# Kernel tuning notes

Measured on AMD Instinct MI355X. Metric: run time of the kernel, lower is better.

Reference implementation:

```python
import jax, jax.numpy as jnp
import numpy as np

N_ATOMS = 10000
N_PAIRS = 500000
N_DESC = 64


def setup_inputs() -> dict:
    key = jax.random.key(0)
    k = jax.random.split(key, 6)
    stdv = float(np.sqrt(6.0 / 3.0))  # matches reset_parameters uniform bound
    return {
        "coeffs": jax.random.normal(k[0], (1, N_ATOMS, N_DESC), dtype=jnp.float32),
        "coeffs_derivs": jax.random.normal(k[1], (1, 3, N_PAIRS, N_DESC), dtype=jnp.float32),
        "w1": jax.random.uniform(k[2], (N_DESC,), jnp.float32, -stdv, stdv),
        "b1": jnp.zeros((N_DESC,), jnp.float32),
        "w_last": jax.random.uniform(k[3], (N_DESC,), jnp.float32, -stdv, stdv),
        "b_last": jnp.zeros((1,), jnp.float32),
        "central_atom_index": jax.random.randint(k[4], (N_PAIRS,), 0, N_ATOMS, dtype=jnp.int32),
        "neigh_atom_index": jax.random.randint(k[5], (N_PAIRS,), 0, N_ATOMS, dtype=jnp.int32),
    }


def reference(coeffs, coeffs_derivs, w1, b1, w_last, b_last,
              central_atom_index, neigh_atom_index):
    # coeffs: [1, N, D]; coeffs_derivs: [1, 3, P, D]
    num_atoms = coeffs.shape[1]
    e_pa = jnp.tanh(coeffs * w1 + b1)            # [1, N, D]
    dfdw = 1.0 - e_pa * e_pa                     # tanh' chain, [1, N, D]
    # gather per-pair central-atom derivative, broadcast over 3 force dims
    f = dfdw[:, central_atom_index, :][:, None, :, :] * (coeffs_derivs * w1)  # [1,3,P,D]
    energy = jnp.sum(e_pa * w_last) / num_atoms + b_last   # [1]
    f = -jnp.sum(f * w_last, axis=3)             # [1, 3, P]
    # scatter-sum pair forces onto neighbor atoms (replaces O(n^2) python loop)
    out_f = jnp.zeros((1, 3, num_atoms), dtype=f.dtype).at[:, :, neigh_atom_index].add(f)
    return energy, out_f
```

## Files before the change

### kernel.cpp

```cpp
#include <hip/hip_runtime.h>

#define N_ATOMS 10000
#define N_PAIRS 500000
#define N_DESC  64

__global__ void init_out_kernel(float* __restrict__ out,
                                const float* __restrict__ b_last,
                                int out_size) {
    int i = blockIdx.x * blockDim.x + threadIdx.x;
    if (i < out_size) out[i] = (i == 0) ? b_last[0] : 0.0f;
}

__global__ void atom_kernel(const float* __restrict__ coeffs,
                            const float* __restrict__ w1,
                            const float* __restrict__ b1,
                            const float* __restrict__ w_last,
                            float* __restrict__ g,
                            float* __restrict__ out) {
    const int i = blockIdx.x * blockDim.x + threadIdx.x;
    const int d = i & (N_DESC - 1);

    const float wd = w1[d];
    const float wl = w_last[d];
    const float e  = tanhf(coeffs[i] * wd + b1[d]);

    g[i] = (1.0f - e * e) * wd * wl;

    float epart = e * wl * (1.0f / (float)N_ATOMS);

    #pragma unroll
    for (int off = 32; off > 0; off >>= 1)
        epart += __shfl_down(epart, off, 64);

    __shared__ float smem[4];
    const int lane = threadIdx.x & 63;
    const int wv   = threadIdx.x >> 6;
    if (lane == 0) smem[wv] = epart;
    __syncthreads();
    if (threadIdx.x == 0) {
        atomicAdd(out, smem[0] + smem[1] + smem[2] + smem[3]);
    }
}

__global__ void __launch_bounds__(256)
pair_kernel(const float4* __restrict__ cd4,
            const float4* __restrict__ g4,
            const int*   __restrict__ central,
            const int*   __restrict__ neigh,
            float* __restrict__ out_f) {
    const int tid = blockIdx.x * blockDim.x + threadIdx.x;
    const int p   = tid >> 4;
    const int l   = tid & 15;
    if (p >= N_PAIRS) return;

    const int c = central[p];
    const float4 gv = g4[c * 16 + l];

    const size_t plane4 = (size_t)N_PAIRS * 16;
    const float4* base = cd4 + (size_t)p * 16 + l;
    const float4 b0 = base[0];
    const float4 b1v = base[plane4];
    const float4 b2 = base[2 * plane4];

    float s0 = gv.x * b0.x  + gv.y * b0.y  + gv.z * b0.z  + gv.w * b0.w;
    float s1 = gv.x * b1v.x + gv.y * b1v.y + gv.z * b1v.z + gv.w * b1v.w;
    float s2 = gv.x * b2.x  + gv.y * b2.y  + gv.z * b2.z  + gv.w * b2.w;

    #pragma unroll
    for (int m = 8; m > 0; m >>= 1) {
        s0 += __shfl_xor(s0, m, 64);
        s1 += __shfl_xor(s1, m, 64);
        s2 += __shfl_xor(s2, m, 64);
    }

    if (l == 0) {
        const int nb = neigh[p];
        atomicAdd(&out_f[nb],               -s0);
        atomicAdd(&out_f[N_ATOMS + nb],     -s1);
        atomicAdd(&out_f[2 * N_ATOMS + nb], -s2);
    }
}

extern "C" void kernel_launch(void* const* d_in, const int* in_sizes, int n_in,
                              void* d_out, int out_size, void* d_ws, size_t ws_size,
                              hipStream_t stream) {
    const float* coeffs  = (const float*)d_in[0];
    const float* cd      = (const float*)d_in[1];
    const float* w1      = (const float*)d_in[2];
    const float* b1      = (const float*)d_in[3];
    const float* w_last  = (const float*)d_in[4];
    const float* b_last  = (const float*)d_in[5];
    const int*   central = (const int*)d_in[6];
    const int*   neigh   = (const int*)d_in[7];

    float* out = (float*)d_out;
    float* g   = (float*)d_ws;

    {
        int blocks = (out_size + 255) / 256;
        init_out_kernel<<<blocks, 256, 0, stream>>>(out, b_last, out_size);
    }

    {
        int total  = N_ATOMS * N_DESC;
        int blocks = total / 256;
        atom_kernel<<<blocks, 256, 0, stream>>>(coeffs, w1, b1, w_last, g, out);
    }

    {
        long long total_threads = (long long)N_PAIRS * 16;
        int blocks = (int)((total_threads + 255) / 256);
        pair_kernel<<<blocks, 256, 0, stream>>>(
            (const float4*)cd, (const float4*)g, central, neigh, out + 1);
    }
}
```

Measured before the change: 546.7 us.

## Fuse output init into atom kernel, process two pairs per thread, spread atomics

Drops the separate init kernel: the atom kernel zeroes the force buffer and writes per-block energy partials to workspace, and the pair kernel's block 0 reduces those partials deterministically. Each 16-lane group now handles two pairs (p and p+P/2) with nontemporal streaming loads, giving more memory-level parallelism per thread. The three atomic adds per pair are spread across different lanes. The aim is less launch overhead, less cache pollution from the large derivative stream, and more loads in flight, at the cost of fewer threads and more registers.

New measurement: 510.5 us. 1.07x faster.

```diff
diff --git a/kernel.cpp b/kernel.cpp
--- a/kernel.cpp
+++ b/kernel.cpp
@@ -3,20 +3,26 @@
 #define N_ATOMS 10000
 #define N_PAIRS 500000
 #define N_DESC  64
+#define HALF_PAIRS (N_PAIRS / 2)
+#define ATOM_BLOCKS (N_ATOMS * N_DESC / 256)
+#define FORCE_ELEMS (3 * N_ATOMS)
 
-__global__ void init_out_kernel(float* __restrict__ out,
-                                const float* __restrict__ b_last,
-                                int out_size) {
-    int i = blockIdx.x * blockDim.x + threadIdx.x;
-    if (i < out_size) out[i] = (i == 0) ? b_last[0] : 0.0f;
-}
+#define WS_EPART_OFF (N_ATOMS * N_DESC)
 
-__global__ void atom_kernel(const float* __restrict__ coeffs,
-                            const float* __restrict__ w1,
-                            const float* __restrict__ b1,
-                            const float* __restrict__ w_last,
-                            float* __restrict__ g,
-                            float* __restrict__ out) {
+typedef float f4 __attribute__((ext_vector_type(4)));
+
+__global__ void __launch_bounds__(256)
+atom_kernel(const float* __restrict__ coeffs,
+            const float* __restrict__ w1,
+            const float* __restrict__ b1,
+            const float* __restrict__ w_last,
+            float* __restrict__ ws,
+            float* __restrict__ out) {
+    if (blockIdx.x < 118) {
+        int j = blockIdx.x * 256 + threadIdx.x;
+        if (j < FORCE_ELEMS) out[1 + j] = 0.0f;
+    }
+
     const int i = blockIdx.x * blockDim.x + threadIdx.x;
     const int d = i & (N_DESC - 1);
 
@@ -24,10 +30,9 @@
     const float wl = w_last[d];
     const float e  = tanhf(coeffs[i] * wd + b1[d]);
 
-    g[i] = (1.0f - e * e) * wd * wl;
+    ws[i] = (1.0f - e * e) * wd * wl;
 
     float epart = e * wl * (1.0f / (float)N_ATOMS);
-
     #pragma unroll
     for (int off = 32; off > 0; off >>= 1)
         epart += __shfl_down(epart, off, 64);
@@ -37,47 +42,82 @@
     const int wv   = threadIdx.x >> 6;
     if (lane == 0) smem[wv] = epart;
     __syncthreads();
-    if (threadIdx.x == 0) {
-        atomicAdd(out, smem[0] + smem[1] + smem[2] + smem[3]);
-    }
+    if (threadIdx.x == 0)
+        ws[WS_EPART_OFF + blockIdx.x] = smem[0] + smem[1] + smem[2] + smem[3];
 }
 
 __global__ void __launch_bounds__(256)
-pair_kernel(const float4* __restrict__ cd4,
-            const float4* __restrict__ g4,
-            const int*   __restrict__ central,
-            const int*   __restrict__ neigh,
-            float* __restrict__ out_f) {
+pair_kernel(const f4* __restrict__ cd4,
+            const f4* __restrict__ g4,
+            const float*  __restrict__ ws,
+            const float*  __restrict__ b_last,
+            const int*    __restrict__ central,
+            const int*    __restrict__ neigh,
+            float* __restrict__ out) {
+    if (blockIdx.x == 0 && threadIdx.x < 64) {
+        float s = 0.0f;
+        for (int idx = threadIdx.x; idx < ATOM_BLOCKS; idx += 64)
+            s += ws[WS_EPART_OFF + idx];
+        #pragma unroll
+        for (int off = 32; off > 0; off >>= 1)
+            s += __shfl_down(s, off, 64);
+        if (threadIdx.x == 0) out[0] = s + b_last[0];
+    }
+
+    float* __restrict__ out_f = out + 1;
+
     const int tid = blockIdx.x * blockDim.x + threadIdx.x;
-    const int p   = tid >> 4;
+    const int grp = tid >> 4;
     const int l   = tid & 15;
-    if (p >= N_PAIRS) return;
+    if (grp >= HALF_PAIRS) return;
 
-    const int c = central[p];
-    const float4 gv = g4[c * 16 + l];
+    const int pA = grp;
+    const int pB = grp + HALF_PAIRS;
+
+    const int cA = central[pA];
+    const int cB = central[pB];
+    const int nA = neigh[pA];
+    const int nB = neigh[pB];
 
     const size_t plane4 = (size_t)N_PAIRS * 16;
-    const float4* base = cd4 + (size_t)p * 16 + l;
-    const float4 b0 = base[0];
-    const float4 b1v = base[plane4];
-    const float4 b2 = base[2 * plane4];
+    const f4* baseA = cd4 + (size_t)pA * 16 + l;
+    const f4* baseB = cd4 + (size_t)pB * 16 + l;
 
-    float s0 = gv.x * b0.x  + gv.y * b0.y  + gv.z * b0.z  + gv.w * b0.w;
-    float s1 = gv.x * b1v.x + gv.y * b1v.y + gv.z * b1v.z + gv.w * b1v.w;
-    float s2 = gv.x * b2.x  + gv.y * b2.y  + gv.z * b2.z  + gv.w * b2.w;
+    const f4 a0 = __builtin_nontemporal_load(baseA);
+    const f4 a1 = __builtin_nontemporal_load(baseA + plane4);
+    const f4 a2 = __builtin_nontemporal_load(baseA + 2 * plane4);
+    const f4 c0 = __builtin_nontemporal_load(baseB);
+    const f4 c1 = __builtin_nontemporal_load(baseB + plane4);
+    const f4 c2 = __builtin_nontemporal_load(baseB + 2 * plane4);
+    const f4 gA = g4[cA * 16 + l];
+    const f4 gB = g4[cB * 16 + l];
+
+    float sA0 = gA.x * a0.x + gA.y * a0.y + gA.z * a0.z + gA.w * a0.w;
+    float sA1 = gA.x * a1.x + gA.y * a1.y + gA.z * a1.z + gA.w * a1.w;
+    float sA2 = gA.x * a2.x + gA.y * a2.y + gA.z * a2.z + gA.w * a2.w;
+    float sB0 = gB.x * c0.x + gB.y * c0.y + gB.z * c0.z + gB.w * c0.w;
+    float sB1 = gB.x * c1.x + gB.y * c1.y + gB.z * c1.z + gB.w * c1.w;
+    float sB2 = gB.x * c2.x + gB.y * c2.y + gB.z * c2.z + gB.w * c2.w;
 
     #pragma unroll
     for (int m = 8; m > 0; m >>= 1) {
-        s0 += __shfl_xor(s0, m, 64);
-        s1 += __shfl_xor(s1, m, 64);
-        s2 += __shfl_xor(s2, m, 64);
+        sA0 += __shfl_xor(sA0, m, 64);
+        sA1 += __shfl_xor(sA1, m, 64);
+        sA2 += __shfl_xor(sA2, m, 64);
+        sB0 += __shfl_xor(sB0, m, 64);
+        sB1 += __shfl_xor(sB1, m, 64);
+        sB2 += __shfl_xor(sB2, m, 64);
     }
 
     if (l == 0) {
-        const int nb = neigh[p];
-        atomicAdd(&out_f[nb],               -s0);
-        atomicAdd(&out_f[N_ATOMS + nb],     -s1);
-        atomicAdd(&out_f[2 * N_ATOMS + nb], -s2);
+        atomicAdd(&out_f[nA], -sA0);
+        atomicAdd(&out_f[nB], -sB0);
+    } else if (l == 4) {
+        atomicAdd(&out_f[N_ATOMS + nA], -sA1);
+        atomicAdd(&out_f[N_ATOMS + nB], -sB1);
+    } else if (l == 8) {
+        atomicAdd(&out_f[2 * N_ATOMS + nA], -sA2);
+        atomicAdd(&out_f[2 * N_ATOMS + nB], -sB2);
     }
 }
 
@@ -94,23 +134,14 @@
     const int*   neigh   = (const int*)d_in[7];
 
     float* out = (float*)d_out;
-    float* g   = (float*)d_ws;
+    float* ws  = (float*)d_ws;
+
+    atom_kernel<<<ATOM_BLOCKS, 256, 0, stream>>>(coeffs, w1, b1, w_last, ws, out);
 
     {
-        int blocks = (out_size + 255) / 256;
-        init_out_kernel<<<blocks, 256, 0, stream>>>(out, b_last, out_size);
-    }
-
-    {
-        int total  = N_ATOMS * N_DESC;
-        int blocks = total / 256;
-        atom_kernel<<<blocks, 256, 0, stream>>>(coeffs, w1, b1, w_last, g, out);
-    }
-
-    {
-        long long total_threads = (long long)N_PAIRS * 16;
+        long long total_threads = (long long)HALF_PAIRS * 16;
         int blocks = (int)((total_threads + 255) / 256);
         pair_kernel<<<blocks, 256, 0, stream>>>(
-            (const float4*)cd, (const float4*)g, central, neigh, out + 1);
+            (const f4*)cd, (const f4*)ws, ws, b_last, central, neigh, out);
     }
 }
```
